# Kernel optimization log

Hardware: AMD Instinct MI355X
Metric: run time of the kernel (lower is better)

The kernel has to match this reference:

```python
import jax, jax.numpy as jnp
import numpy as np

NUM_SEGMENTS = 100000
N = 33554432

def setup_inputs() -> dict:
    key = jax.random.key(0)
    k1, k2 = jax.random.split(key)
    x = jax.random.normal(k1, (N,), dtype=jnp.float32)
    index = jnp.sort(jax.random.randint(k2, (N,), 0, NUM_SEGMENTS, dtype=jnp.int64))
    return {"x": x, "index": index}

def reference(x, index):
    # segment sum and count, then mean with clamp(min=1) on the count
    seg_sum = jax.ops.segment_sum(x, index, num_segments=NUM_SEGMENTS)
    seg_cnt = jax.ops.segment_sum(jnp.ones_like(x), index, num_segments=NUM_SEGMENTS)
    return seg_sum / jnp.maximum(seg_cnt, 1.0)
```

## Files before the change

### kernel.cpp

```cpp
#include <hip/hip_runtime.h>


#define NSEG 100000

__global__ __launch_bounds__(256) void bounds_kernel(
    const int* __restrict__ index, int n, int* __restrict__ seg_start) {
    int s = blockIdx.x * blockDim.x + threadIdx.x;
    if (s > NSEG) return;
    int lo = 0, hi = n;
    while (lo < hi) {
        int mid = (lo + hi) >> 1;
        if (index[mid] < s) lo = mid + 1; else hi = mid;
    }
    seg_start[s] = lo;
}

__global__ __launch_bounds__(256) void segsum_kernel(
    const float* __restrict__ x, const int* __restrict__ seg_start,
    float* __restrict__ out) {
    int wave_id = (int)((blockIdx.x * blockDim.x + threadIdx.x) >> 6);
    int lane = threadIdx.x & 63;
    if (wave_id >= NSEG) return;

    int beg = seg_start[wave_id];
    int end = seg_start[wave_id + 1];

    float sum = 0.0f;
    for (int i = beg + lane; i < end; i += 64) sum += x[i];

    #pragma unroll
    for (int off = 32; off > 0; off >>= 1) sum += __shfl_down(sum, off, 64);

    if (lane == 0) {
        int cnt = end - beg;
        out[wave_id] = sum / (float)(cnt > 0 ? cnt : 1);
    }
}

extern "C" void kernel_launch(void* const* d_in, const int* in_sizes, int n_in,
                              void* d_out, int out_size, void* d_ws, size_t ws_size,
                              hipStream_t stream) {
    const float* x   = (const float*)d_in[0];
    const int*   idx = (const int*)d_in[1];
    float*       out = (float*)d_out;
    int n = in_sizes[0];

    int* seg_start = (int*)d_ws;

    {
        int threads = 256;
        int blocks = (NSEG + 1 + threads - 1) / threads;
        bounds_kernel<<<blocks, threads, 0, stream>>>(idx, n, seg_start);
    }

    {
        int threads = 256;
        int waves_per_block = threads / 64;
        int blocks = (NSEG + waves_per_block - 1) / waves_per_block;
        segsum_kernel<<<blocks, threads, 0, stream>>>(x, seg_start, out);
    }
}
```

Measured before the change: 284.6 us.

## Fuse segment-bound search into mean kernel and vectorize loads with float4

Merges the binary-search bounds kernel into the segment-sum kernel: lanes 0 and 1 of each wave binary-search the start and end of their segment and broadcast them with shuffles. This removes one kernel launch and the workspace round trip. The main sum loop now reads aligned float4 chunks, with scalar loads for the unaligned head and tail. The cost is two serial binary searches per wave on the critical path before the streaming loads begin, so each segment now does twice as many searches as before.

```diff
diff --git a/kernel.cpp b/kernel.cpp
--- a/kernel.cpp
+++ b/kernel.cpp
@@ -3,37 +3,47 @@
 
 #define NSEG 100000
 
-__global__ __launch_bounds__(256) void bounds_kernel(
-    const int* __restrict__ index, int n, int* __restrict__ seg_start) {
-    int s = blockIdx.x * blockDim.x + threadIdx.x;
-    if (s > NSEG) return;
-    int lo = 0, hi = n;
-    while (lo < hi) {
-        int mid = (lo + hi) >> 1;
-        if (index[mid] < s) lo = mid + 1; else hi = mid;
+__global__ __launch_bounds__(256) void meanpool_fused(
+    const float* __restrict__ x, const int* __restrict__ index, int n,
+    float* __restrict__ out) {
+    int wid  = (int)((blockIdx.x * (unsigned)blockDim.x + threadIdx.x) >> 6);
+    int lane = threadIdx.x & 63;
+    if (wid >= NSEG) return;
+
+    int bound = 0;
+    if (lane < 2) {
+        int target = wid + lane;
+        int lo = 0, hi = n;
+        while (lo < hi) {
+            int mid = (lo + hi) >> 1;
+            if (index[mid] < target) lo = mid + 1; else hi = mid;
+        }
+        bound = lo;
     }
-    seg_start[s] = lo;
-}
-
-__global__ __launch_bounds__(256) void segsum_kernel(
-    const float* __restrict__ x, const int* __restrict__ seg_start,
-    float* __restrict__ out) {
-    int wave_id = (int)((blockIdx.x * blockDim.x + threadIdx.x) >> 6);
-    int lane = threadIdx.x & 63;
-    if (wave_id >= NSEG) return;
-
-    int beg = seg_start[wave_id];
-    int end = seg_start[wave_id + 1];
+    int beg = __shfl(bound, 0, 64);
+    int end = __shfl(bound, 1, 64);
 
     float sum = 0.0f;
-    for (int i = beg + lane; i < end; i += 64) sum += x[i];
+    int beg4 = (beg + 3) & ~3;
+    int end4 = end & ~3;
+
+    if (end4 <= beg4) {
+        for (int i = beg + lane; i < end; i += 64) sum += x[i];
+    } else {
+        if (lane < (beg4 - beg)) sum += x[beg + lane];
+        for (int i = beg4 + lane * 4; i < end4; i += 64 * 4) {
+            float4 v = *reinterpret_cast<const float4*>(x + i);
+            sum += v.x + v.y + v.z + v.w;
+        }
+        if (lane < (end - end4)) sum += x[end4 + lane];
+    }
 
     #pragma unroll
     for (int off = 32; off > 0; off >>= 1) sum += __shfl_down(sum, off, 64);
 
     if (lane == 0) {
         int cnt = end - beg;
-        out[wave_id] = sum / (float)(cnt > 0 ? cnt : 1);
+        out[wid] = sum / (float)(cnt > 0 ? cnt : 1);
     }
 }
 
@@ -45,18 +55,8 @@
     float*       out = (float*)d_out;
     int n = in_sizes[0];
 
-    int* seg_start = (int*)d_ws;
-
-    {
-        int threads = 256;
-        int blocks = (NSEG + 1 + threads - 1) / threads;
-        bounds_kernel<<<blocks, threads, 0, stream>>>(idx, n, seg_start);
-    }
-
-    {
-        int threads = 256;
-        int waves_per_block = threads / 64;
-        int blocks = (NSEG + waves_per_block - 1) / waves_per_block;
-        segsum_kernel<<<blocks, threads, 0, stream>>>(x, seg_start, out);
-    }
+    int threads = 256;
+    int waves_per_block = threads / 64;
+    int blocks = (NSEG + waves_per_block - 1) / waves_per_block;
+    meanpool_fused<<<blocks, threads, 0, stream>>>(x, idx, n, out);
 }
```

Measured after the change: 390.7 us. +37.3%, slower.
